# Kernel optimization log

Measured on AMD Instinct MI355X. Metric: run time of the kernel, lower is better.

## Reference

```python
import jax, jax.numpy as jnp
import numpy as np

MAX_SENTS = 20  # sentences 0..19 are real; id == MAX_SENTS means token in no sentence


def setup_inputs() -> dict:
    key = jax.random.key(0)
    k1, k2 = jax.random.split(key)
    B, S, D = 64, 512, 768
    hidden = jax.random.normal(k1, (B, S, D), dtype=jnp.float32)
    # token -> sentence id; MAX_SENTS marks tokens (CLS/SEP/pad) outside any sentence
    sent_ids = jax.random.randint(k2, (B, S), 0, MAX_SENTS + 1, dtype=jnp.int32)
    return {"hidden": hidden, "sent_ids": sent_ids, "max_sents": MAX_SENTS}


def reference(hidden, sent_ids, max_sents):
    # hidden: [B, S, D] BERT last_hidden_state; sent_ids: [B, S] token->sentence id.
    B, S, D = hidden.shape
    M1 = max_sents + 1  # extra bucket for non-sentence tokens
    doc_cls_reps = hidden[:, 0, :]  # [B, D]
    # Fused segment-sum over flattened (batch, sentence) segments.
    flat_ids = (jnp.arange(B, dtype=sent_ids.dtype)[:, None] * M1 + sent_ids).reshape(-1)
    sums = jax.ops.segment_sum(hidden.reshape(B * S, D), flat_ids, num_segments=B * M1)
    counts = jax.ops.segment_sum(jnp.ones((B * S,), dtype=hidden.dtype), flat_ids,
                                 num_segments=B * M1)
    sums = sums.reshape(B, M1, D)[:, :max_sents]          # drop invalid bucket
    counts = counts.reshape(B, M1)[:, :max_sents]
    # mean with clamp(min=1) on counts, as in the torch code
    sent_reps = sums / jnp.clip(counts, 1.0, None)[:, :, None]  # [B, max_sents, D]
    return doc_cls_reps, sent_reps
```

## Files before the change

kernel.cpp:

```cpp
#include <hip/hip_runtime.h>


constexpr int B_ = 64;
constexpr int S_ = 512;
constexpr int D_ = 768;
constexpr int M1 = 21;
constexpr int MS = 20;
constexpr int CF = 256;
constexpr int NC = D_ / CF;
constexpr int G  = 16;
constexpr int RPW = S_ / G;
constexpr int P  = 8;

__global__ __launch_bounds__(64 * G, 1)
void aspire_kernel(const float* __restrict__ hidden,
                   const int* __restrict__ sent_ids,
                   float* __restrict__ out) {
    __shared__ float acc[M1 * CF];
    __shared__ int   cnt[M1];
    __shared__ int   offs[M1];
    __shared__ short ord[S_];
    __shared__ short ssid[S_];
    __shared__ int   sids[S_];

    const int b    = blockIdx.x;
    const int dc   = blockIdx.y;
    const int lane = threadIdx.x;
    const int g    = threadIdx.y;
    const int tid  = g * 64 + lane;

    for (int i = tid; i < M1 * CF; i += 64 * G) acc[i] = 0.0f;
    if (tid < M1) cnt[tid] = 0;
    __syncthreads();
    if (tid < S_) {
        int sv = sent_ids[b * S_ + tid];
        sids[tid] = sv;
        atomicAdd(&cnt[sv], 1);
    }
    __syncthreads();
    if (tid == 0) {
        int r = 0;
        for (int k = 0; k < M1; ++k) { offs[k] = r; r += cnt[k]; }
    }
    __syncthreads();
    if (tid < S_) {
        int sv  = sids[tid];
        int pos = atomicAdd(&offs[sv], 1);
        ord[pos]  = (short)tid;
        ssid[pos] = (short)sv;
    }
    if (tid < CF) {
        out[b * D_ + dc * CF + tid] = hidden[(size_t)b * S_ * D_ + dc * CF + tid];
    }
    __syncthreads();

    const float* hb = hidden + (size_t)b * S_ * D_ + dc * CF + 4 * lane;
    const int p0 = g * RPW;

    float4 buf[P];
    #pragma unroll
    for (int j = 0; j < P; ++j) {
        int s = ord[p0 + j];
        buf[j] = *(const float4*)(hb + (size_t)s * D_);
    }

    float sx = 0.0f, sy = 0.0f, sz = 0.0f, sw = 0.0f;
    int cur = ssid[p0];

    #pragma unroll 1
    for (int t0 = 0; t0 < RPW - P; t0 += P) {
        #pragma unroll
        for (int j = 0; j < P; ++j) {
            int t   = t0 + j;
            int sid = ssid[p0 + t];
            if (sid != cur) {
                float* a = &acc[cur * CF + 4 * lane];
                atomicAdd(a + 0, sx);
                atomicAdd(a + 1, sy);
                atomicAdd(a + 2, sz);
                atomicAdd(a + 3, sw);
                sx = sy = sz = sw = 0.0f;
                cur = sid;
            }
            float4 v = buf[j];
            sx += v.x; sy += v.y; sz += v.z; sw += v.w;
            int sn = ord[p0 + t + P];
            buf[j] = *(const float4*)(hb + (size_t)sn * D_);
        }
    }
    #pragma unroll
    for (int j = 0; j < P; ++j) {
        int t   = RPW - P + j;
        int sid = ssid[p0 + t];
        if (sid != cur) {
            float* a = &acc[cur * CF + 4 * lane];
            atomicAdd(a + 0, sx);
            atomicAdd(a + 1, sy);
            atomicAdd(a + 2, sz);
            atomicAdd(a + 3, sw);
            sx = sy = sz = sw = 0.0f;
            cur = sid;
        }
        float4 v = buf[j];
        sx += v.x; sy += v.y; sz += v.z; sw += v.w;
    }
    {
        float* a = &acc[cur * CF + 4 * lane];
        atomicAdd(a + 0, sx);
        atomicAdd(a + 1, sy);
        atomicAdd(a + 2, sz);
        atomicAdd(a + 3, sw);
    }
    __syncthreads();

    float* srep = out + (size_t)B_ * D_;
    for (int f = tid; f < MS * CF; f += 64 * G) {
        int seg = f / CF;
        int col = f - seg * CF;
        float ct = (float)cnt[seg];
        ct = ct < 1.0f ? 1.0f : ct;
        srep[((size_t)b * MS + seg) * D_ + dc * CF + col] =
            acc[seg * CF + col] / ct;
    }
}

extern "C" void kernel_launch(void* const* d_in, const int* in_sizes, int n_in,
                              void* d_out, int out_size, void* d_ws, size_t ws_size,
                              hipStream_t stream) {
    const float* hidden   = (const float*)d_in[0];
    const int*   sent_ids = (const int*)d_in[1];
    float* out = (float*)d_out;

    dim3 grid(B_, NC);
    dim3 block(64, G);
    aspire_kernel<<<grid, block, 0, stream>>>(hidden, sent_ids, out);
}
```

Baseline: 153.3 us.

## Split sequence across blocks with workspace partials and a separate reduce kernel

Each (batch, feature-chunk) block is split into four sequence chunks, each run by a 256-thread block, raising the grid from 192 to 768 blocks and allowing several blocks per CU. Partial sums go to a global workspace and a second kernel adds the partials and divides by the clamped counts. This aims to fix under-occupancy of the GPU, at the cost of extra workspace traffic (about 16MB written and read) and a second kernel launch.

```diff
diff --git a/kernel.cpp b/kernel.cpp
--- a/kernel.cpp
+++ b/kernel.cpp
@@ -1,61 +1,73 @@
 #include <hip/hip_runtime.h>
 
 
-constexpr int B_ = 64;
-constexpr int S_ = 512;
-constexpr int D_ = 768;
-constexpr int M1 = 21;
-constexpr int MS = 20;
-constexpr int CF = 256;
-constexpr int NC = D_ / CF;
-constexpr int G  = 16;
-constexpr int RPW = S_ / G;
-constexpr int P  = 8;
+constexpr int B_  = 64;
+constexpr int S_  = 512;
+constexpr int D_  = 768;
+constexpr int M1  = 21;
+constexpr int MS  = 20;
+constexpr int CF  = 256;
+constexpr int NC  = 3;
+constexpr int NSC = 4;
+constexpr int SC  = S_ / NSC;
+constexpr int NT  = 256;
+constexpr int NW  = 4;
+constexpr int RPW = SC / NW;
+constexpr int P   = 8;
 
-__global__ __launch_bounds__(64 * G, 1)
-void aspire_kernel(const float* __restrict__ hidden,
-                   const int* __restrict__ sent_ids,
-                   float* __restrict__ out) {
+constexpr size_t WS_PART = (size_t)B_ * NSC * MS * D_;
+
+__global__ __launch_bounds__(NT, 3)
+void aspire_main(const float* __restrict__ hidden,
+                 const int* __restrict__ sent_ids,
+                 float* __restrict__ out,
+                 float* __restrict__ ws) {
     __shared__ float acc[M1 * CF];
+    __shared__ int   sids[S_];
     __shared__ int   cnt[M1];
-    __shared__ int   offs[M1];
-    __shared__ short ord[S_];
-    __shared__ short ssid[S_];
-    __shared__ int   sids[S_];
+    __shared__ int   ccnt[M1];
+    __shared__ int   coffs[M1];
+    __shared__ short ord[SC];
+    __shared__ short ssid[SC];
 
     const int b    = blockIdx.x;
     const int dc   = blockIdx.y;
-    const int lane = threadIdx.x;
-    const int g    = threadIdx.y;
-    const int tid  = g * 64 + lane;
+    const int sc   = blockIdx.z;
+    const int tid  = threadIdx.x;
+    const int lane = tid & 63;
+    const int w    = tid >> 6;
 
-    for (int i = tid; i < M1 * CF; i += 64 * G) acc[i] = 0.0f;
-    if (tid < M1) cnt[tid] = 0;
+    for (int i = tid; i < M1 * CF; i += NT) acc[i] = 0.0f;
+    if (tid < M1) { cnt[tid] = 0; ccnt[tid] = 0; }
     __syncthreads();
-    if (tid < S_) {
-        int sv = sent_ids[b * S_ + tid];
-        sids[tid] = sv;
+
+    for (int i = tid; i < S_; i += NT) {
+        int sv = sent_ids[b * S_ + i];
+        sids[i] = sv;
         atomicAdd(&cnt[sv], 1);
     }
     __syncthreads();
+
+    if (tid < SC) atomicAdd(&ccnt[sids[sc * SC + tid]], 1);
+    __syncthreads();
     if (tid == 0) {
         int r = 0;
-        for (int k = 0; k < M1; ++k) { offs[k] = r; r += cnt[k]; }
+        for (int k = 0; k < M1; ++k) { coffs[k] = r; r += ccnt[k]; }
     }
     __syncthreads();
-    if (tid < S_) {
-        int sv  = sids[tid];
-        int pos = atomicAdd(&offs[sv], 1);
+    if (tid < SC) {
+        int sv  = sids[sc * SC + tid];
+        int pos = atomicAdd(&coffs[sv], 1);
         ord[pos]  = (short)tid;
         ssid[pos] = (short)sv;
     }
-    if (tid < CF) {
+    if (sc == 0) {
         out[b * D_ + dc * CF + tid] = hidden[(size_t)b * S_ * D_ + dc * CF + tid];
     }
     __syncthreads();
 
-    const float* hb = hidden + (size_t)b * S_ * D_ + dc * CF + 4 * lane;
-    const int p0 = g * RPW;
+    const float* hb = hidden + ((size_t)b * S_ + sc * SC) * D_ + dc * CF + 4 * lane;
+    const int p0 = w * RPW;
 
     float4 buf[P];
     #pragma unroll
@@ -75,10 +87,8 @@
             int sid = ssid[p0 + t];
             if (sid != cur) {
                 float* a = &acc[cur * CF + 4 * lane];
-                atomicAdd(a + 0, sx);
-                atomicAdd(a + 1, sy);
-                atomicAdd(a + 2, sz);
-                atomicAdd(a + 3, sw);
+                atomicAdd(a + 0, sx); atomicAdd(a + 1, sy);
+                atomicAdd(a + 2, sz); atomicAdd(a + 3, sw);
                 sx = sy = sz = sw = 0.0f;
                 cur = sid;
             }
@@ -94,10 +104,8 @@
         int sid = ssid[p0 + t];
         if (sid != cur) {
             float* a = &acc[cur * CF + 4 * lane];
-            atomicAdd(a + 0, sx);
-            atomicAdd(a + 1, sy);
-            atomicAdd(a + 2, sz);
-            atomicAdd(a + 3, sw);
+            atomicAdd(a + 0, sx); atomicAdd(a + 1, sy);
+            atomicAdd(a + 2, sz); atomicAdd(a + 3, sw);
             sx = sy = sz = sw = 0.0f;
             cur = sid;
         }
@@ -106,22 +114,44 @@
     }
     {
         float* a = &acc[cur * CF + 4 * lane];
-        atomicAdd(a + 0, sx);
-        atomicAdd(a + 1, sy);
-        atomicAdd(a + 2, sz);
-        atomicAdd(a + 3, sw);
+        atomicAdd(a + 0, sx); atomicAdd(a + 1, sy);
+        atomicAdd(a + 2, sz); atomicAdd(a + 3, sw);
     }
     __syncthreads();
 
-    float* srep = out + (size_t)B_ * D_;
-    for (int f = tid; f < MS * CF; f += 64 * G) {
-        int seg = f / CF;
-        int col = f - seg * CF;
-        float ct = (float)cnt[seg];
-        ct = ct < 1.0f ? 1.0f : ct;
-        srep[((size_t)b * MS + seg) * D_ + dc * CF + col] =
-            acc[seg * CF + col] / ct;
+    for (int f = tid; f < MS * CF; f += NT) {
+        int seg = f >> 8;
+        int col = f & (CF - 1);
+        ws[((size_t)(b * NSC + sc) * MS + seg) * D_ + dc * CF + col] =
+            acc[seg * CF + col];
     }
+    if (dc == 0 && sc == 0 && tid < MS) {
+        ws[WS_PART + b * MS + tid] = (float)cnt[tid];
+    }
+}
+
+__global__ __launch_bounds__(NT)
+void aspire_reduce(const float* __restrict__ ws, float* __restrict__ out) {
+    int i = blockIdx.x * NT + threadIdx.x;
+    if (i >= (B_ * MS * D_) / 4) return;
+    int e0   = i * 4;
+    int bseg = e0 / D_;
+    int d    = e0 - bseg * D_;
+    int b    = bseg / MS;
+    int seg  = bseg - b * MS;
+
+    float4 s = {0.f, 0.f, 0.f, 0.f};
+    #pragma unroll
+    for (int scn = 0; scn < NSC; ++scn) {
+        const float4 p = *(const float4*)
+            (ws + ((size_t)(b * NSC + scn) * MS + seg) * D_ + d);
+        s.x += p.x; s.y += p.y; s.z += p.z; s.w += p.w;
+    }
+    float ct = ws[WS_PART + bseg];
+    ct = ct < 1.0f ? 1.0f : ct;
+    float inv = 1.0f / ct;
+    float4 r = {s.x * inv, s.y * inv, s.z * inv, s.w * inv};
+    *(float4*)(out + (size_t)B_ * D_ + e0) = r;
 }
 
 extern "C" void kernel_launch(void* const* d_in, const int* in_sizes, int n_in,
@@ -130,8 +160,11 @@
     const float* hidden   = (const float*)d_in[0];
     const int*   sent_ids = (const int*)d_in[1];
     float* out = (float*)d_out;
+    float* ws  = (float*)d_ws;
 
-    dim3 grid(B_, NC);
-    dim3 block(64, G);
-    aspire_kernel<<<grid, block, 0, stream>>>(hidden, sent_ids, out);
+    dim3 grid(B_, NC, NSC);
+    aspire_main<<<grid, NT, 0, stream>>>(hidden, sent_ids, out, ws);
+
+    int n4 = (B_ * MS * D_) / 4;
+    aspire_reduce<<<n4 / NT, NT, 0, stream>>>(ws, out);
 }
```

After: 162.9 us. 6.3% more time.
